# Optimization experiments

Measured on AMD Instinct MI355X. Metric: run time of the kernel, lower is better.

The kernel has to match this reference:

```python
import jax, jax.numpy as jnp
import numpy as np

HIDDEN = 256
NUM_REL = 6
NUM_BASES = 30
N_NODES = 50000
N_EDGES = 800000


def rgcn_gate_layer(x, src, dst, etype, basis, att, root, bias, gate_w, gate_b):
    # Basis-decomposed relation weights: W_r = sum_b att[r,b] * basis[b]
    N = x.shape[0]
    W = jnp.einsum('rb,bio->rio', att, basis)           # [R, d, d]
    # Transform all nodes under every relation (cheaper than per-edge matmul
    # since N*R < E), then gather the per-edge message.
    xw = jnp.einsum('nd,rde->rne', x, W)                # [R, N, d]
    msg = xw[etype, src]                                # [E, d]
    # Scalar sigmoid gate per edge message
    g = jax.nn.sigmoid(msg @ gate_w + gate_b)           # [E, 1]
    gated = g * msg
    # Mean aggregation over incoming edges per destination node
    agg = jax.ops.segment_sum(gated, dst, num_segments=N)
    deg = jax.ops.segment_sum(jnp.ones((src.shape[0], 1), x.dtype), dst,
                              num_segments=N)
    agg = agg / jnp.maximum(deg, 1.0)
    return agg + x @ root + bias


def setup_inputs() -> dict:
    key = jax.random.key(0)
    ks = jax.random.split(key, 16)
    d = HIDDEN
    inp = {
        'x': jax.random.normal(ks[0], (N_NODES, d), jnp.float32),
        'edge_src': jax.random.randint(ks[1], (N_EDGES,), 0, N_NODES, jnp.int32),
        'edge_dst': jax.random.randint(ks[2], (N_EDGES,), 0, N_NODES, jnp.int32),
        'edge_type': jax.random.randint(ks[3], (N_EDGES,), 0, NUM_REL, jnp.int32),
    }
    def glorot(k, shape):
        fan = shape[-2] + shape[-1]
        return jax.random.uniform(k, shape, jnp.float32,
                                  -np.sqrt(6.0 / fan), np.sqrt(6.0 / fan))
    for li, off in ((1, 4), (2, 10)):
        inp[f'basis{li}'] = glorot(ks[off + 0], (NUM_BASES, d, d))
        inp[f'att{li}'] = glorot(ks[off + 1], (NUM_REL, NUM_BASES))
        inp[f'root{li}'] = glorot(ks[off + 2], (d, d))
        inp[f'bias{li}'] = jnp.zeros((d,), jnp.float32)
        inp[f'gate_w{li}'] = glorot(ks[off + 3], (d, 1))
        inp[f'gate_b{li}'] = jnp.zeros((1,), jnp.float32)
    return inp


def reference(x, edge_src, edge_dst, edge_type,
              basis1, att1, root1, bias1, gate_w1, gate_b1,
              basis2, att2, root2, bias2, gate_w2, gate_b2):
    h = jax.nn.relu(rgcn_gate_layer(x, edge_src, edge_dst, edge_type,
                                    basis1, att1, root1, bias1,
                                    gate_w1, gate_b1))
    out = rgcn_gate_layer(h, edge_src, edge_dst, edge_type,
                          basis2, att2, root2, bias2, gate_w2, gate_b2)
    return out
```

## Files before the change

### kernel.cpp

```cpp
#include <hip/hip_runtime.h>
#include <cmath>

#define HIDDEN 256
#define NUM_REL 6
#define KA 1536
#define KB 1792

typedef float f32x4_t __attribute__((ext_vector_type(4)));
typedef short bf16x8_t __attribute__((ext_vector_type(8)));

__device__ __forceinline__ float bf2f(ushort u) {
  return __uint_as_float(((uint)u) << 16);
}
__device__ __forceinline__ ushort f2bf(float f) {
  uint u = __float_as_uint(f);
  u += 0x7FFFu + ((u >> 16) & 1u);
  return (ushort)(u >> 16);
}

__global__ void compute_W_kernel(const float* __restrict__ att,
                                 const float* __restrict__ basis,
                                 float* __restrict__ Wall) {
  int idx = blockIdx.x * blockDim.x + threadIdx.x;
  int r  = idx >> 16;
  int io = idx & 65535;
  float s = 0.f;
#pragma unroll
  for (int b = 0; b < 30; ++b)
    s += att[r * 30 + b] * basis[(size_t)b * 65536 + io];
  Wall[idx] = s;
}

__global__ __launch_bounds__(256) void gatevec_kernel(
    const float* __restrict__ Wall, const float* __restrict__ gw,
    float* __restrict__ gatevec) {
  const int wave = (blockIdx.x * blockDim.x + threadIdx.x) >> 6;
  const int l = threadIdx.x & 63;
  const int r = wave >> 8, d = wave & 255;
  float4 wv = ((const float4*)(Wall + (size_t)r * 65536 + d * 256))[l];
  float4 gv = ((const float4*)gw)[l];
  float dot = wv.x * gv.x + wv.y * gv.y + wv.z * gv.z + wv.w * gv.w;
#pragma unroll
  for (int off = 32; off; off >>= 1) dot += __shfl_xor(dot, off);
  if (l == 0) gatevec[r * 256 + d] = dot;
}

__global__ __launch_bounds__(256) void build_BT2(const float* __restrict__ Wall,
                                                 const float* __restrict__ root,
                                                 ushort* __restrict__ BT2) {
  __shared__ float t[64][65];
  const int o0 = blockIdx.x * 64, k0 = blockIdx.y * 64, r = blockIdx.z;
  const float* S = (r < 6) ? (Wall + (size_t)r * 65536) : root;
  const int tx = threadIdx.x & 63, ty = threadIdx.x >> 6;
  for (int kk = ty; kk < 64; kk += 4)
    t[kk][tx] = S[(size_t)(k0 + kk) * 256 + o0 + tx];
  __syncthreads();
  for (int oo = ty; oo < 64; oo += 4)
    BT2[(size_t)(o0 + oo) * KB + r * 256 + k0 + tx] = f2bf(t[tx][oo]);
}

__global__ void cvt_f32_bf16(const float* __restrict__ in,
                             ushort* __restrict__ out, int n4) {
  int i = blockIdx.x * blockDim.x + threadIdx.x;
  if (i >= n4) return;
  float4 v = ((const float4*)in)[i];
  ushort4 o;
  o.x = f2bf(v.x); o.y = f2bf(v.y); o.z = f2bf(v.z); o.w = f2bf(v.w);
  ((ushort4*)out)[i] = o;
}

__global__ __launch_bounds__(256) void gdot_kernel(
    const ushort* __restrict__ xb, const float* __restrict__ gatevec,
    const float* __restrict__ gate_b, float* __restrict__ G, int N) {
  const int wave = (blockIdx.x * blockDim.x + threadIdx.x) >> 6;
  if (wave >= N) return;
  const int l = threadIdx.x & 63;
  ushort4 xv = ((const ushort4*)(xb + (size_t)wave * 256))[l];
  const float x0 = bf2f(xv.x), x1 = bf2f(xv.y), x2 = bf2f(xv.z), x3 = bf2f(xv.w);
  float out = 0.f;
#pragma unroll
  for (int r = 0; r < NUM_REL; ++r) {
    float4 gv = ((const float4*)(gatevec + r * 256))[l];
    float d = x0 * gv.x + x1 * gv.y + x2 * gv.z + x3 * gv.w;
#pragma unroll
    for (int off = 32; off; off >>= 1) d += __shfl_xor(d, off);
    if (l == r) out = d;
  }
  if (l < NUM_REL) {
    const float gb = gate_b[0];
    G[(size_t)l * N + wave] = 1.f / (1.f + __expf(-(out + gb)));
  }
}

#define ACCUM(rj, gj, vj)                                                  \
  do {                                                                    \
    const float fx = (gj)*bf2f((vj).x), fy = (gj)*bf2f((vj).y);           \
    const float fz = (gj)*bf2f((vj).z), fw = (gj)*bf2f((vj).w);           \
    switch (rj) {                                                         \
      case 0: a0x += fx; a0y += fy; a0z += fz; a0w += fw; break;          \
      case 1: a1x += fx; a1y += fy; a1z += fz; a1w += fw; break;          \
      case 2: a2x += fx; a2y += fy; a2z += fz; a2w += fw; break;          \
      case 3: a3x += fx; a3y += fy; a3z += fz; a3w += fw; break;          \
      case 4: a4x += fx; a4y += fy; a4z += fz; a4w += fw; break;          \
      default: a5x += fx; a5y += fy; a5z += fz; a5w += fw; break;         \
    }                                                                     \
  } while (0)

__global__ __launch_bounds__(256) void edge_agg(
    const ushort* __restrict__ xb, const float* __restrict__ G,
    const int* __restrict__ rp8, const int* __restrict__ src_s,
    ushort* __restrict__ A, int N) {
  const int n = (blockIdx.x * blockDim.x + threadIdx.x) >> 6;
  if (n >= N) return;
  const int l = threadIdx.x & 63;
  const int b0 = rp8[n * 8 + 0], b1 = rp8[n * 8 + 1], b2 = rp8[n * 8 + 2];
  const int b3 = rp8[n * 8 + 3], b4 = rp8[n * 8 + 4], b5 = rp8[n * 8 + 5];
  const int b6 = rp8[n * 8 + 6];

  float a0x = 0, a0y = 0, a0z = 0, a0w = 0, a1x = 0, a1y = 0, a1z = 0, a1w = 0;
  float a2x = 0, a2y = 0, a2z = 0, a2w = 0, a3x = 0, a3y = 0, a3z = 0, a3w = 0;
  float a4x = 0, a4y = 0, a4z = 0, a4w = 0, a5x = 0, a5y = 0, a5z = 0, a5w = 0;

  int e = b0;
  for (; e + 3 < b6; e += 4) {
    const int s0 = src_s[e], s1 = src_s[e + 1];
    const int s2 = src_s[e + 2], s3 = src_s[e + 3];
    const ushort4 v0 = ((const ushort4*)(xb + (size_t)s0 * 256))[l];
    const ushort4 v1 = ((const ushort4*)(xb + (size_t)s1 * 256))[l];
    const ushort4 v2 = ((const ushort4*)(xb + (size_t)s2 * 256))[l];
    const ushort4 v3 = ((const ushort4*)(xb + (size_t)s3 * 256))[l];
    const int r0 = (e >= b1) + (e >= b2) + (e >= b3) + (e >= b4) + (e >= b5);
    const int e1i = e + 1, e2i = e + 2, e3i = e + 3;
    const int r1 = (e1i >= b1) + (e1i >= b2) + (e1i >= b3) + (e1i >= b4) + (e1i >= b5);
    const int r2 = (e2i >= b1) + (e2i >= b2) + (e2i >= b3) + (e2i >= b4) + (e2i >= b5);
    const int r3 = (e3i >= b1) + (e3i >= b2) + (e3i >= b3) + (e3i >= b4) + (e3i >= b5);
    const float g0 = G[(size_t)r0 * N + s0];
    const float g1 = G[(size_t)r1 * N + s1];
    const float g2 = G[(size_t)r2 * N + s2];
    const float g3 = G[(size_t)r3 * N + s3];
    ACCUM(r0, g0, v0); ACCUM(r1, g1, v1);
    ACCUM(r2, g2, v2); ACCUM(r3, g3, v3);
  }
  for (; e < b6; ++e) {
    const int s0 = src_s[e];
    const ushort4 v0 = ((const ushort4*)(xb + (size_t)s0 * 256))[l];
    const int r0 = (e >= b1) + (e >= b2) + (e >= b3) + (e >= b4) + (e >= b5);
    const float g0 = G[(size_t)r0 * N + s0];
    ACCUM(r0, g0, v0);
  }

  const float inv = 1.f / fmaxf((float)(b6 - b0), 1.f);
  ushort* Arow = A + (size_t)n * KA;
  ushort4 o;
  o.x = f2bf(a0x * inv); o.y = f2bf(a0y * inv); o.z = f2bf(a0z * inv); o.w = f2bf(a0w * inv);
  ((ushort4*)(Arow + 0 * 256))[l] = o;
  o.x = f2bf(a1x * inv); o.y = f2bf(a1y * inv); o.z = f2bf(a1z * inv); o.w = f2bf(a1w * inv);
  ((ushort4*)(Arow + 1 * 256))[l] = o;
  o.x = f2bf(a2x * inv); o.y = f2bf(a2y * inv); o.z = f2bf(a2z * inv); o.w = f2bf(a2w * inv);
  ((ushort4*)(Arow + 2 * 256))[l] = o;
  o.x = f2bf(a3x * inv); o.y = f2bf(a3y * inv); o.z = f2bf(a3z * inv); o.w = f2bf(a3w * inv);
  ((ushort4*)(Arow + 3 * 256))[l] = o;
  o.x = f2bf(a4x * inv); o.y = f2bf(a4y * inv); o.z = f2bf(a4z * inv); o.w = f2bf(a4w * inv);
  ((ushort4*)(Arow + 4 * 256))[l] = o;
  o.x = f2bf(a5x * inv); o.y = f2bf(a5y * inv); o.z = f2bf(a5z * inv); o.w = f2bf(a5w * inv);
  ((ushort4*)(Arow + 5 * 256))[l] = o;
}

__global__ __launch_bounds__(256) void gemm_fused(const ushort* __restrict__ A,
                                                  const ushort* __restrict__ xb,
                                                  const ushort* __restrict__ BT,
                                                  const float* __restrict__ bias,
                                                  void* __restrict__ outPtr,
                                                  int M, int mode) {
  __shared__ ushort As[128 * 64];
  __shared__ ushort Bs[128 * 64];
  const int mB = (M + 127) >> 7;
  const int bid = blockIdx.x;
  const int yb = (bid >> 4) * 8 + (bid & 7);
  if (yb >= mB) return;
  const int col0 = ((bid >> 3) & 1) * 128;
  const int row0 = yb * 128;

  const int tid = threadIdx.x;
  const int w = tid >> 6, l = tid & 63;
  const int wm = w & 1, wn = w >> 1;

  const int srow = l >> 3;
  const int schunk = (l & 7) ^ srow;

  f32x4_t acc[4][4] = {};

  for (int k0 = 0; k0 < KB; k0 += 64) {
    if (k0) __syncthreads();
#pragma unroll
    for (int i = 0; i < 4; ++i) {
      const int br = (w * 4 + i) * 8;
      const int ga = min(row0 + br + srow, M - 1);
      const ushort* gp = (k0 < KA)
          ? (A + (size_t)ga * KA + k0 + schunk * 8)
          : (xb + (size_t)ga * 256 + (k0 - KA) + schunk * 8);
      __builtin_amdgcn_global_load_lds(
          (const __attribute__((address_space(1))) void*)gp,
          (__attribute__((address_space(3))) void*)(As + br * 64), 16, 0, 0);
    }
#pragma unroll
    for (int i = 0; i < 4; ++i) {
      const int br = (w * 4 + i) * 8;
      const int gb = col0 + br + srow;
      const ushort* gp = BT + (size_t)gb * KB + k0 + schunk * 8;
      __builtin_amdgcn_global_load_lds(
          (const __attribute__((address_space(1))) void*)gp,
          (__attribute__((address_space(3))) void*)(Bs + br * 64), 16, 0, 0);
    }
    __syncthreads();
#pragma unroll
    for (int kk = 0; kk < 2; ++kk) {
      const int swc = (kk * 4 + (l >> 4)) ^ (l & 7);
      bf16x8_t a[4], b[4];
#pragma unroll
      for (int m = 0; m < 4; ++m) {
        const int r = wm * 64 + m * 16 + (l & 15);
        a[m] = *(const bf16x8_t*)(As + r * 64 + swc * 8);
      }
#pragma unroll
      for (int n = 0; n < 4; ++n) {
        const int r = wn * 64 + n * 16 + (l & 15);
        b[n] = *(const bf16x8_t*)(Bs + r * 64 + swc * 8);
      }
#pragma unroll
      for (int m = 0; m < 4; ++m)
#pragma unroll
        for (int n = 0; n < 4; ++n)
          acc[m][n] = __builtin_amdgcn_mfma_f32_16x16x32_bf16(
              a[m], b[n], acc[m][n], 0, 0, 0);
    }
  }

  const int rbase = row0 + wm * 64 + (l >> 4) * 4;
  const int cbase = col0 + wn * 64 + (l & 15);
#pragma unroll
  for (int n = 0; n < 4; ++n) {
    const int col = cbase + n * 16;
    const float bv = bias[col];
#pragma unroll
    for (int m = 0; m < 4; ++m)
#pragma unroll
      for (int i = 0; i < 4; ++i) {
        const int row = rbase + m * 16 + i;
        if (row < M) {
          float v = acc[m][n][i] + bv;
          if (mode == 0) {
            v = fmaxf(v, 0.f);
            ((ushort*)outPtr)[(size_t)row * 256 + col] = f2bf(v);
          } else {
            ((float*)outPtr)[(size_t)row * 256 + col] = v;
          }
        }
      }
  }
}

__global__ void hist_kernel(const int* __restrict__ dst,
                            const int* __restrict__ ety,
                            int* __restrict__ cnt, int E) {
  int stride = gridDim.x * blockDim.x;
  for (int e = blockIdx.x * blockDim.x + threadIdx.x; e < E; e += stride)
    atomicAdd(&cnt[dst[e] * 8 + ety[e]], 1);
}

__global__ void scan_reduce(const int* __restrict__ cnt,
                            int* __restrict__ blockSums, int n) {
  __shared__ int sd[256];
  int base = blockIdx.x * 1024;
  int t = threadIdx.x;
  int s = 0;
#pragma unroll
  for (int i = 0; i < 4; ++i) {
    int idx = base + t * 4 + i;
    s += (idx < n) ? cnt[idx] : 0;
  }
  sd[t] = s; __syncthreads();
  for (int off = 128; off; off >>= 1) {
    if (t < off) sd[t] += sd[t + off];
    __syncthreads();
  }
  if (t == 0) blockSums[blockIdx.x] = sd[0];
}

__global__ void scan_offsets(int* __restrict__ blockSums, int nb) {
  __shared__ int sd[512];
  const int t = threadIdx.x;
  const int v = (t < nb) ? blockSums[t] : 0;
  sd[t] = v; __syncthreads();
  for (int off = 1; off < 512; off <<= 1) {
    int u = (t >= off) ? sd[t - off] : 0;
    __syncthreads();
    sd[t] += u;
    __syncthreads();
  }
  if (t < nb) blockSums[t] = sd[t] - v;
}

__global__ void scan_write(const int* __restrict__ cnt,
                           const int* __restrict__ blockSums,
                           int* __restrict__ row_ptr, int n) {
  __shared__ int sd[256];
  int base = blockIdx.x * 1024;
  int t = threadIdx.x;
  int v[4]; int s = 0;
#pragma unroll
  for (int i = 0; i < 4; ++i) {
    int idx = base + t * 4 + i;
    v[i] = (idx < n) ? cnt[idx] : 0;
    s += v[i];
  }
  sd[t] = s; __syncthreads();
  for (int off = 1; off < 256; off <<= 1) {
    int val = (t >= off) ? sd[t - off] : 0;
    __syncthreads();
    sd[t] += val;
    __syncthreads();
  }
  int excl = blockSums[blockIdx.x] + sd[t] - s;
  for (int i = 0; i < 4; ++i) {
    int idx = base + t * 4 + i;
    if (idx < n) {
      row_ptr[idx] = excl;
      excl += v[i];
      if (idx == n - 1) row_ptr[n] = excl;
    }
  }
}

__global__ void scatter_kernel(const int* __restrict__ src,
                               const int* __restrict__ dst,
                               const int* __restrict__ ety,
                               int* __restrict__ cursor,
                               int* __restrict__ src_s, int E) {
  int stride = gridDim.x * blockDim.x;
  for (int e = blockIdx.x * blockDim.x + threadIdx.x; e < E; e += stride) {
    int bin = dst[e] * 8 + ety[e];
    int pos = atomicAdd(&cursor[bin], 1);
    src_s[pos] = src[e];
  }
}

static inline size_t align16(size_t x) { return (x + 15) & ~(size_t)15; }

extern "C" void kernel_launch(void* const* d_in, const int* in_sizes, int n_in,
                              void* d_out, int out_size, void* d_ws,
                              size_t ws_size, hipStream_t stream) {
  const float* x    = (const float*)d_in[0];
  const int*   src  = (const int*)d_in[1];
  const int*   dst  = (const int*)d_in[2];
  const int*   ety  = (const int*)d_in[3];

  const int N   = in_sizes[0] / HIDDEN;
  const int E   = in_sizes[1];
  const int RN2 = N * 8;

  char* p = (char*)d_ws;
  float* Wall    = (float*)p;  p += align16((size_t)NUM_REL * 65536 * 4);
  ushort* BT2    = (ushort*)p; p += align16((size_t)256 * KB * 2);
  float* gatevec = (float*)p;  p += align16((size_t)NUM_REL * 256 * 4);
  float* G       = (float*)p;  p += align16((size_t)NUM_REL * N * 4);
  ushort* xb0    = (ushort*)p; p += align16((size_t)N * HIDDEN * 2);
  ushort* xb1    = (ushort*)p; p += align16((size_t)N * HIDDEN * 2);
  int* cnt       = (int*)p;    p += align16((size_t)RN2 * 4);
  int* cursor    = (int*)p;    p += align16((size_t)RN2 * 4);
  int* row_ptr   = (int*)p;    p += align16((size_t)(RN2 + 1) * 4);
  int* blockSums = (int*)p;    p += 2048;
  int* src_s     = (int*)p;    p += align16((size_t)E * 4);
  ushort* A      = (ushort*)p;

  const int scanBlocks = (RN2 + 1023) / 1024;

  hipMemsetAsync(cnt, 0, (size_t)RN2 * sizeof(int), stream);
  hist_kernel<<<2048, 256, 0, stream>>>(dst, ety, cnt, E);
  scan_reduce<<<scanBlocks, 256, 0, stream>>>(cnt, blockSums, RN2);
  scan_offsets<<<1, 512, 0, stream>>>(blockSums, scanBlocks);
  scan_write<<<scanBlocks, 256, 0, stream>>>(cnt, blockSums, row_ptr, RN2);
  hipMemcpyAsync(cursor, row_ptr, (size_t)RN2 * sizeof(int),
                 hipMemcpyDeviceToDevice, stream);
  scatter_kernel<<<2048, 256, 0, stream>>>(src, dst, ety, cursor, src_s, E);

  cvt_f32_bf16<<<(N * 64 + 255) / 256, 256, 0, stream>>>(x, xb0, N * 64);

  const int nodeBlocks = (N * 64 + 255) / 256;
  const int mBlocks = (N + 127) / 128;
  const int gemmGrid = ((mBlocks + 7) / 8) * 16;

  for (int layer = 0; layer < 2; ++layer) {
    const float* bas  = (const float*)d_in[layer ? 10 : 4];
    const float* att  = (const float*)d_in[layer ? 11 : 5];
    const float* root = (const float*)d_in[layer ? 12 : 6];
    const float* bias = (const float*)d_in[layer ? 13 : 7];
    const float* gw   = (const float*)d_in[layer ? 14 : 8];
    const float* gb   = (const float*)d_in[layer ? 15 : 9];
    const ushort* xb  = layer ? xb1 : xb0;
    void* outp = layer ? d_out : (void*)xb1;
    const int mode = layer ? 1 : 0;

    compute_W_kernel<<<NUM_REL * 65536 / 256, 256, 0, stream>>>(att, bas, Wall);
    gatevec_kernel<<<384, 256, 0, stream>>>(Wall, gw, gatevec);
    build_BT2<<<dim3(4, 4, 7), 256, 0, stream>>>(Wall, root, BT2);
    gdot_kernel<<<nodeBlocks, 256, 0, stream>>>(xb, gatevec, gb, G, N);
    edge_agg<<<nodeBlocks, 256, 0, stream>>>(xb, G, row_ptr, src_s, A, N);
    gemm_fused<<<gemmGrid, 256, 0, stream>>>(A, xb, BT2, bias, outp, N, mode);
  }
}
```

Measured before the change: 564.7 us.

## Triple-buffer A tiles in GEMM, stream B fragments from registers, unroll edge gather

The GEMM now keeps three LDS buffers for the A tile and issues loads two k-steps ahead, replacing the two __syncthreads per step with a vmcnt wait and a single barrier. B is pre-packed into a fragment-ordered layout (build_BTf), so each wave reads its MFMA operands straight from global memory into registers and double-buffers them, which removes B from LDS. The edge aggregation loop is unrolled from 4 to 8 edges to keep more gathers in flight. The cost is higher register pressure and a hand-tuned waitcnt count that must stay in step with the number of loads issued per stage.

Measured after the change: 542.8 us. 1.04x faster.

```diff
diff --git a/kernel.cpp b/kernel.cpp
--- a/kernel.cpp
+++ b/kernel.cpp
@@ -5,6 +5,9 @@
 #define NUM_REL 6
 #define KA 1536
 #define KB 1792
+#define NKSTEP 28
+#define KASTEP 24
+#define CTSTRIDE 28672
 
 typedef float f32x4_t __attribute__((ext_vector_type(4)));
 typedef short bf16x8_t __attribute__((ext_vector_type(8)));
@@ -45,18 +48,18 @@
   if (l == 0) gatevec[r * 256 + d] = dot;
 }
 
-__global__ __launch_bounds__(256) void build_BT2(const float* __restrict__ Wall,
-                                                 const float* __restrict__ root,
-                                                 ushort* __restrict__ BT2) {
-  __shared__ float t[64][65];
-  const int o0 = blockIdx.x * 64, k0 = blockIdx.y * 64, r = blockIdx.z;
-  const float* S = (r < 6) ? (Wall + (size_t)r * 65536) : root;
-  const int tx = threadIdx.x & 63, ty = threadIdx.x >> 6;
-  for (int kk = ty; kk < 64; kk += 4)
-    t[kk][tx] = S[(size_t)(k0 + kk) * 256 + o0 + tx];
-  __syncthreads();
-  for (int oo = ty; oo < 64; oo += 4)
-    BT2[(size_t)(o0 + oo) * KB + r * 256 + k0 + tx] = f2bf(t[tx][oo]);
+__global__ void build_BTf(const float* __restrict__ Wall,
+                          const float* __restrict__ root,
+                          ushort* __restrict__ BTf) {
+  int tid = blockIdx.x * blockDim.x + threadIdx.x;
+  if (tid >= KB * 256) return;
+  int o = tid & 255, gk = tid >> 8;
+  int r = gk >> 8, kin = gk & 255;
+  float v = (r < 6) ? Wall[(size_t)r * 65536 + kin * 256 + o]
+                    : root[(size_t)kin * 256 + o];
+  size_t idx = (size_t)(o >> 4) * CTSTRIDE + (size_t)(gk >> 3) * 128 +
+               (o & 15) * 8 + (gk & 7);
+  BTf[idx] = f2bf(v);
 }
 
 __global__ void cvt_f32_bf16(const float* __restrict__ in,
@@ -106,6 +109,8 @@
     }                                                                     \
   } while (0)
 
+#define RELOF(ei) ((ei >= b1) + (ei >= b2) + (ei >= b3) + (ei >= b4) + (ei >= b5))
+
 __global__ __launch_bounds__(256) void edge_agg(
     const ushort* __restrict__ xb, const float* __restrict__ G,
     const int* __restrict__ rp8, const int* __restrict__ src_s,
@@ -122,29 +127,33 @@
   float a4x = 0, a4y = 0, a4z = 0, a4w = 0, a5x = 0, a5y = 0, a5z = 0, a5w = 0;
 
   int e = b0;
-  for (; e + 3 < b6; e += 4) {
-    const int s0 = src_s[e], s1 = src_s[e + 1];
+  for (; e + 7 < b6; e += 8) {
+    const int s0 = src_s[e + 0], s1 = src_s[e + 1];
     const int s2 = src_s[e + 2], s3 = src_s[e + 3];
+    const int s4 = src_s[e + 4], s5 = src_s[e + 5];
+    const int s6 = src_s[e + 6], s7 = src_s[e + 7];
     const ushort4 v0 = ((const ushort4*)(xb + (size_t)s0 * 256))[l];
     const ushort4 v1 = ((const ushort4*)(xb + (size_t)s1 * 256))[l];
     const ushort4 v2 = ((const ushort4*)(xb + (size_t)s2 * 256))[l];
     const ushort4 v3 = ((const ushort4*)(xb + (size_t)s3 * 256))[l];
-    const int r0 = (e >= b1) + (e >= b2) + (e >= b3) + (e >= b4) + (e >= b5);
-    const int e1i = e + 1, e2i = e + 2, e3i = e + 3;
-    const int r1 = (e1i >= b1) + (e1i >= b2) + (e1i >= b3) + (e1i >= b4) + (e1i >= b5);
-    const int r2 = (e2i >= b1) + (e2i >= b2) + (e2i >= b3) + (e2i >= b4) + (e2i >= b5);
-    const int r3 = (e3i >= b1) + (e3i >= b2) + (e3i >= b3) + (e3i >= b4) + (e3i >= b5);
-    const float g0 = G[(size_t)r0 * N + s0];
-    const float g1 = G[(size_t)r1 * N + s1];
-    const float g2 = G[(size_t)r2 * N + s2];
-    const float g3 = G[(size_t)r3 * N + s3];
-    ACCUM(r0, g0, v0); ACCUM(r1, g1, v1);
-    ACCUM(r2, g2, v2); ACCUM(r3, g3, v3);
+    const ushort4 v4 = ((const ushort4*)(xb + (size_t)s4 * 256))[l];
+    const ushort4 v5 = ((const ushort4*)(xb + (size_t)s5 * 256))[l];
+    const ushort4 v6 = ((const ushort4*)(xb + (size_t)s6 * 256))[l];
+    const ushort4 v7 = ((const ushort4*)(xb + (size_t)s7 * 256))[l];
+    const int r0 = RELOF(e + 0), r1 = RELOF(e + 1), r2 = RELOF(e + 2),
+              r3 = RELOF(e + 3), r4 = RELOF(e + 4), r5 = RELOF(e + 5),
+              r6 = RELOF(e + 6), r7 = RELOF(e + 7);
+    const float g0 = G[(size_t)r0 * N + s0], g1 = G[(size_t)r1 * N + s1];
+    const float g2 = G[(size_t)r2 * N + s2], g3 = G[(size_t)r3 * N + s3];
+    const float g4 = G[(size_t)r4 * N + s4], g5 = G[(size_t)r5 * N + s5];
+    const float g6 = G[(size_t)r6 * N + s6], g7 = G[(size_t)r7 * N + s7];
+    ACCUM(r0, g0, v0); ACCUM(r1, g1, v1); ACCUM(r2, g2, v2); ACCUM(r3, g3, v3);
+    ACCUM(r4, g4, v4); ACCUM(r5, g5, v5); ACCUM(r6, g6, v6); ACCUM(r7, g7, v7);
   }
   for (; e < b6; ++e) {
     const int s0 = src_s[e];
     const ushort4 v0 = ((const ushort4*)(xb + (size_t)s0 * 256))[l];
-    const int r0 = (e >= b1) + (e >= b2) + (e >= b3) + (e >= b4) + (e >= b5);
+    const int r0 = RELOF(e);
     const float g0 = G[(size_t)r0 * N + s0];
     ACCUM(r0, g0, v0);
   }
@@ -168,17 +177,16 @@
 
 __global__ __launch_bounds__(256) void gemm_fused(const ushort* __restrict__ A,
                                                   const ushort* __restrict__ xb,
-                                                  const ushort* __restrict__ BT,
+                                                  const ushort* __restrict__ BTf,
                                                   const float* __restrict__ bias,
                                                   void* __restrict__ outPtr,
                                                   int M, int mode) {
-  __shared__ ushort As[128 * 64];
-  __shared__ ushort Bs[128 * 64];
+  __shared__ ushort As[3 * 8192];
   const int mB = (M + 127) >> 7;
   const int bid = blockIdx.x;
   const int yb = (bid >> 4) * 8 + (bid & 7);
   if (yb >= mB) return;
-  const int col0 = ((bid >> 3) & 1) * 128;
+  const int colh = (bid >> 3) & 1;
   const int row0 = yb * 128;
 
   const int tid = threadIdx.x;
@@ -188,56 +196,76 @@
   const int srow = l >> 3;
   const int schunk = (l & 7) ^ srow;
 
+  const ushort* Bbase = BTf + (size_t)(colh * 8 + wn * 4) * CTSTRIDE +
+                        (l >> 4) * 128 + (l & 15) * 8;
+
   f32x4_t acc[4][4] = {};
 
-  for (int k0 = 0; k0 < KB; k0 += 64) {
-    if (k0) __syncthreads();
+  auto stage = [&](int k, int buf) {
+    const int ko = k * 64;
 #pragma unroll
     for (int i = 0; i < 4; ++i) {
       const int br = (w * 4 + i) * 8;
       const int ga = min(row0 + br + srow, M - 1);
-      const ushort* gp = (k0 < KA)
-          ? (A + (size_t)ga * KA + k0 + schunk * 8)
-          : (xb + (size_t)ga * 256 + (k0 - KA) + schunk * 8);
+      const ushort* gp = (k < KASTEP)
+          ? (A + (size_t)ga * KA + ko + schunk * 8)
+          : (xb + (size_t)ga * 256 + (ko - KA) + schunk * 8);
       __builtin_amdgcn_global_load_lds(
           (const __attribute__((address_space(1))) void*)gp,
-          (__attribute__((address_space(3))) void*)(As + br * 64), 16, 0, 0);
+          (__attribute__((address_space(3))) void*)(As + buf * 8192 + br * 64),
+          16, 0, 0);
     }
-#pragma unroll
-    for (int i = 0; i < 4; ++i) {
-      const int br = (w * 4 + i) * 8;
-      const int gb = col0 + br + srow;
-      const ushort* gp = BT + (size_t)gb * KB + k0 + schunk * 8;
-      __builtin_amdgcn_global_load_lds(
-          (const __attribute__((address_space(1))) void*)gp,
-          (__attribute__((address_space(3))) void*)(Bs + br * 64), 16, 0, 0);
-    }
-    __syncthreads();
+  };
+
+  bf16x8_t bc[2][4], bn[2][4];
+
+  stage(0, 0);
+  stage(1, 1);
+#pragma unroll
+  for (int kk = 0; kk < 2; ++kk)
+#pragma unroll
+    for (int n = 0; n < 4; ++n)
+      bc[kk][n] = *(const bf16x8_t*)(Bbase + (size_t)n * CTSTRIDE + kk * 512);
+
+#pragma unroll 2
+  for (int k = 0; k < NKSTEP; ++k) {
+    const int cur = k % 3;
+    asm volatile("s_waitcnt vmcnt(12)" ::: "memory");
+    __builtin_amdgcn_s_barrier();
+#pragma unroll
+    for (int kk = 0; kk < 2; ++kk)
+#pragma unroll
+      for (int n = 0; n < 4; ++n)
+        bn[kk][n] = *(const bf16x8_t*)(Bbase + (size_t)n * CTSTRIDE +
+                                       (size_t)(k + 1) * 1024 + kk * 512);
+    __builtin_amdgcn_sched_barrier(0);
+    if (k + 2 < NKSTEP) stage(k + 2, (k + 2) % 3);
+
 #pragma unroll
     for (int kk = 0; kk < 2; ++kk) {
       const int swc = (kk * 4 + (l >> 4)) ^ (l & 7);
-      bf16x8_t a[4], b[4];
+      bf16x8_t a[4];
 #pragma unroll
       for (int m = 0; m < 4; ++m) {
-        const int r = wm * 64 + m * 16 + (l & 15);
-        a[m] = *(const bf16x8_t*)(As + r * 64 + swc * 8);
-      }
-#pragma unroll
-      for (int n = 0; n < 4; ++n) {
-        const int r = wn * 64 + n * 16 + (l & 15);
-        b[n] = *(const bf16x8_t*)(Bs + r * 64 + swc * 8);
+        const int rr = wm * 64 + m * 16 + (l & 15);
+        a[m] = *(const bf16x8_t*)(As + cur * 8192 + rr * 64 + swc * 8);
       }
 #pragma unroll
       for (int m = 0; m < 4; ++m)
 #pragma unroll
         for (int n = 0; n < 4; ++n)
           acc[m][n] = __builtin_amdgcn_mfma_f32_16x16x32_bf16(
-              a[m], b[n], acc[m][n], 0, 0, 0);
+              a[m], bc[kk][n], acc[m][n], 0, 0, 0);
     }
+#pragma unroll
+    for (int kk = 0; kk < 2; ++kk)
+#pragma unroll
+      for (int n = 0; n < 4; ++n)
+        bc[kk][n] = bn[kk][n];
   }
 
   const int rbase = row0 + wm * 64 + (l >> 4) * 4;
-  const int cbase = col0 + wn * 64 + (l & 15);
+  const int cbase = colh * 128 + wn * 64 + (l & 15);
 #pragma unroll
   for (int n = 0; n < 4; ++n) {
     const int col = cbase + n * 16;
@@ -361,7 +389,7 @@
 
   char* p = (char*)d_ws;
   float* Wall    = (float*)p;  p += align16((size_t)NUM_REL * 65536 * 4);
-  ushort* BT2    = (ushort*)p; p += align16((size_t)256 * KB * 2);
+  ushort* BTf    = (ushort*)p; p += align16(((size_t)16 * CTSTRIDE + 1024) * 2);
   float* gatevec = (float*)p;  p += align16((size_t)NUM_REL * 256 * 4);
   float* G       = (float*)p;  p += align16((size_t)NUM_REL * N * 4);
   ushort* xb0    = (ushort*)p; p += align16((size_t)N * HIDDEN * 2);
@@ -403,9 +431,9 @@
 
     compute_W_kernel<<<NUM_REL * 65536 / 256, 256, 0, stream>>>(att, bas, Wall);
     gatevec_kernel<<<384, 256, 0, stream>>>(Wall, gw, gatevec);
-    build_BT2<<<dim3(4, 4, 7), 256, 0, stream>>>(Wall, root, BT2);
+    build_BTf<<<(KB * 256 + 255) / 256, 256, 0, stream>>>(Wall, root, BTf);
     gdot_kernel<<<nodeBlocks, 256, 0, stream>>>(xb, gatevec, gb, G, N);
     edge_agg<<<nodeBlocks, 256, 0, stream>>>(xb, G, row_ptr, src_s, A, N);
-    gemm_fused<<<gemmGrid, 256, 0, stream>>>(A, xb, BT2, bias, outp, N, mode);
-  }
-}
+    gemm_fused<<<gemmGrid, 256, 0, stream>>>(A, xb, BTf, bias, outp, N, mode);
+  }
+}
```
